# Kernel optimization log

Hardware: AMD Instinct MI355X
Metric: run time of the kernel (lower is better)

The kernel has to match this reference:

```python
import jax, jax.numpy as jnp
import numpy as np

EMBED_DIM = 128
N_EMBED = 10000
INPUT_SHAPE = (8, 64, 32, EMBED_DIM)


def setup_inputs() -> dict:
    key = jax.random.key(0)
    k1, k2 = jax.random.split(key)
    inputs = jax.random.normal(k1, INPUT_SHAPE, dtype=jnp.float32)
    cluster_mean = jax.random.normal(k2, (EMBED_DIM, N_EMBED), dtype=jnp.float32)
    return {"inputs": inputs, "cluster_mean": cluster_mean}


def reference(inputs, cluster_mean):
    embed_dim = cluster_mean.shape[0]
    # Flatten all leading dims: (N, D)
    samples = inputs.reshape(-1, embed_dim)
    # Squared euclidean distance to each code: (N, n_embed)
    dist = (
        jnp.sum(samples ** 2, axis=1, keepdims=True)
        - 2.0 * samples @ cluster_mean
        + jnp.sum(cluster_mean ** 2, axis=0, keepdims=True)
    )
    cluster_index = jnp.argmin(dist, axis=1).reshape(inputs.shape[:-1])
    # Embedding lookup from transposed codebook: (..., D)
    quantize = cluster_mean.T[cluster_index]
    q_loss = jnp.mean((quantize - jax.lax.stop_gradient(inputs)) ** 2)
    e_loss = jnp.mean((jax.lax.stop_gradient(quantize) - inputs) ** 2)
    loss = q_loss + 0.25 * e_loss
    # Straight-through estimator
    outputs = inputs + jax.lax.stop_gradient(quantize - inputs)
    return outputs, loss
```

## Files before the change

### kernel.cpp

```cpp
#include <hip/hip_runtime.h>

#define EMBED 128
#define NCODE 10000
#define NSAMP 16384
#define NCODE_PAD 10240
#define NSPLIT 8
#define SPLIT_CODES 1280
#define NCHUNK 20
#define CHUNK_ELEMS 8192
#define OUT_ELEMS (NSAMP * EMBED)
#define TAU 0.002f
#define NSEG 16

typedef float f32x16 __attribute__((ext_vector_type(16)));
typedef short s16x8 __attribute__((ext_vector_type(8)));
typedef unsigned short ushort_t;
typedef unsigned long long u64;

#define OFF_AH  0
#define OFF_AL  2621440
#define OFF_CT  5242880
#define OFF_CN  10485760
#define OFF_KEY 10526720
#define OFF_C2  11575296
#define OFF_IDX 12099584
#define OFF_RL  12165120
#define OFF_CNT 12230656
#define OFF_BEST 12230720

__device__ __forceinline__ unsigned short f2bf(float f) {
    unsigned u = __float_as_uint(f);
    return (unsigned short)((u + 0x7fffu + ((u >> 16) & 1u)) >> 16);
}
__device__ __forceinline__ float bf2f(unsigned short h) {
    return __uint_as_float(((unsigned)h) << 16);
}
__device__ __forceinline__ unsigned ordf(float f) {
    unsigned u = __float_as_uint(f);
    return (u & 0x80000000u) ? ~u : (u | 0x80000000u);
}
__device__ __forceinline__ float unordf(unsigned o) {
    return __uint_as_float((o & 0x80000000u) ? (o ^ 0x80000000u) : ~o);
}

__global__ __launch_bounds__(256) void prep_all(const float* __restrict__ C,
                                                ushort_t* __restrict__ Ah,
                                                ushort_t* __restrict__ Al,
                                                float* __restrict__ CT,
                                                float* __restrict__ cnorm,
                                                float* __restrict__ out,
                                                int* __restrict__ counter) {
    __shared__ float red[256];
    const int t  = threadIdx.x;
    const int nl = t & 15;
    const int kg = t >> 4;
    const int n  = blockIdx.x * 16 + nl;
    if (blockIdx.x == 0 && t == 0) { out[OUT_ELEMS] = 0.f; *counter = 0; }

    const int split = n / SPLIT_CODES;
    const int rem   = n % SPLIT_CODES;
    const int chunk = rem >> 6;
    const int mb    = (rem >> 5) & 1;
    const int row   = rem & 31;
    const int ks = kg >> 1, kh = kg & 1;
    const size_t eoff = (size_t)(split * NCHUNK + chunk) * CHUNK_ELEMS
                      + (size_t)(mb * 4096 + (ks * 2 + kh) * 256 + row * 8);
    const int k0 = kg * 8;
    float f[8];
    float s = 0.f;
#pragma unroll
    for (int j = 0; j < 8; ++j) {
        f[j] = (n < NCODE) ? C[(size_t)(k0 + j) * NCODE + n] : 0.f;
        s = fmaf(f[j], f[j], s);
    }
    *(float4*)(CT + (size_t)n * EMBED + k0)     = make_float4(f[0], f[1], f[2], f[3]);
    *(float4*)(CT + (size_t)n * EMBED + k0 + 4) = make_float4(f[4], f[5], f[6], f[7]);
    s16x8 vh, vl;
#pragma unroll
    for (int j = 0; j < 8; ++j) {
        unsigned short h = f2bf(f[j]);
        vh[j] = (short)h;
        vl[j] = (short)f2bf(f[j] - bf2f(h));
    }
    *(s16x8*)(Ah + eoff) = vh;
    *(s16x8*)(Al + eoff) = vl;

    red[t] = s;
    __syncthreads();
    if (t < 128) red[t] += red[t + 128];
    __syncthreads();
    if (t < 64) red[t] += red[t + 64];
    __syncthreads();
    if (t < 32) red[t] += red[t + 32];
    __syncthreads();
    if (t < 16) {
        const int nn = blockIdx.x * 16 + t;
        cnorm[nn] = (nn < NCODE) ? (red[t] + red[t + 16]) : 3.0e38f;
    }
}

__global__ __launch_bounds__(256, 2) void vq7(const float* __restrict__ X,
                                              const ushort_t* __restrict__ Ah,
                                              const ushort_t* __restrict__ Al,
                                              const float* __restrict__ cnorm,
                                              u64* __restrict__ candKey,
                                              unsigned* __restrict__ cand2) {
    __shared__ ushort_t Bs[2 * 2 * CHUNK_ELEMS];
    __shared__ __align__(16) float cns[SPLIT_CODES];
    const int t    = threadIdx.x;
    const int lane = t & 63;
    const int wave = t >> 6;
    const int ln   = lane & 31;
    const int kh   = lane >> 5;
    const int split = blockIdx.y;
    const int m0    = blockIdx.x * 256;
    const int sbase = split * SPLIT_CODES;

    s16x8 bh[2][8], bl[2][8];
#pragma unroll
    for (int g = 0; g < 2; ++g) {
        int m = m0 + wave * 64 + g * 32 + ln;
#pragma unroll
        for (int ks = 0; ks < 8; ++ks) {
            const float* src = X + (size_t)m * EMBED + ks * 16 + kh * 8;
            float4 f0 = *(const float4*)src;
            float4 f1 = *(const float4*)(src + 4);
            float f[8] = {f0.x, f0.y, f0.z, f0.w, f1.x, f1.y, f1.z, f1.w};
            s16x8 vh, vl;
#pragma unroll
            for (int j = 0; j < 8; ++j) {
                float v = -2.f * f[j];
                unsigned short h = f2bf(v);
                vh[j] = (short)h;
                vl[j] = (short)f2bf(v - bf2f(h));
            }
            bh[g][ks] = vh;
            bl[g][ks] = vl;
        }
    }

    for (int i = t; i < SPLIT_CODES; i += 256) cns[i] = cnorm[sbase + i];

    float v1[2] = {3.4e38f, 3.4e38f}, v2[2] = {3.4e38f, 3.4e38f};
    int   j1[2] = {0, 0};

    auto ldsw = (__attribute__((address_space(3))) ushort_t*)Bs;
    const int woff = wave * 2048;
    const size_t chbase = (size_t)(split * NCHUNK) * CHUNK_ELEMS;

    auto stage = [&](int cc, int buf) {
        const size_t sb = chbase + (size_t)cc * CHUNK_ELEMS;
        const ushort_t* sh = Ah + sb + woff + lane * 8;
        const ushort_t* sl = Al + sb + woff + lane * 8;
        const int db = buf * 2 * CHUNK_ELEMS + woff;
#pragma unroll
        for (int i = 0; i < 4; ++i) {
            __builtin_amdgcn_global_load_lds(
                (const __attribute__((address_space(1))) void*)(sh + i * 512),
                (__attribute__((address_space(3))) void*)(ldsw + db + i * 512),
                16, 0, 0);
            __builtin_amdgcn_global_load_lds(
                (const __attribute__((address_space(1))) void*)(sl + i * 512),
                (__attribute__((address_space(3))) void*)(ldsw + db + CHUNK_ELEMS + i * 512),
                16, 0, 0);
        }
    };

#define MFMA_PHASE(BB, MB, CB2, P0, P1)                                       \
    {                                                                         \
        const float4 q0 = *(const float4*)&cns[(CB2)];                        \
        const float4 q1 = *(const float4*)&cns[(CB2) + 8];                    \
        const float4 q2 = *(const float4*)&cns[(CB2) + 16];                   \
        const float4 q3 = *(const float4*)&cns[(CB2) + 24];                   \
        P0 = (f32x16){q0.x, q0.y, q0.z, q0.w, q1.x, q1.y, q1.z, q1.w,         \
                      q2.x, q2.y, q2.z, q2.w, q3.x, q3.y, q3.z, q3.w};        \
        P1 = P0;                                                              \
        _Pragma("unroll")                                                     \
        for (int ks = 0; ks < 8; ++ks) {                                      \
            const int fo = (BB) + (MB) * 4096 + (ks * 2 + kh) * 256 + ln * 8; \
            s16x8 a_h = *(const s16x8*)&Bs[fo];                               \
            s16x8 a_l = *(const s16x8*)&Bs[CHUNK_ELEMS + fo];                 \
            P0 = __builtin_amdgcn_mfma_f32_32x32x16_bf16(a_h, bh[0][ks], P0, 0, 0, 0); \
            P1 = __builtin_amdgcn_mfma_f32_32x32x16_bf16(a_h, bh[1][ks], P1, 0, 0, 0); \
            P0 = __builtin_amdgcn_mfma_f32_32x32x16_bf16(a_h, bl[0][ks], P0, 0, 0, 0); \
            P1 = __builtin_amdgcn_mfma_f32_32x32x16_bf16(a_h, bl[1][ks], P1, 0, 0, 0); \
            P0 = __builtin_amdgcn_mfma_f32_32x32x16_bf16(a_l, bh[0][ks], P0, 0, 0, 0); \
            P1 = __builtin_amdgcn_mfma_f32_32x32x16_bf16(a_l, bh[1][ks], P1, 0, 0, 0); \
        }                                                                     \
    }

#define EPI(P0, P1, CB2)                                                      \
    {                                                                         \
        _Pragma("unroll")                                                     \
        for (int r = 0; r < 16; ++r) {                                        \
            const int cc = (CB2) + ((r & 3) + 8 * (r >> 2));                  \
            const float d0 = P0[r];                                           \
            if (d0 < v1[0]) j1[0] = cc;                                       \
            v2[0] = fminf(v2[0], fmaxf(d0, v1[0]));                           \
            v1[0] = fminf(v1[0], d0);                                         \
            const float d1 = P1[r];                                           \
            if (d1 < v1[1]) j1[1] = cc;                                       \
            v2[1] = fminf(v2[1], fmaxf(d1, v1[1]));                           \
            v1[1] = fminf(v1[1], d1);                                         \
        }                                                                     \
    }

    f32x16 aA0, aA1, aB0, aB1;
    int cbA, cbB;

    stage(0, 0);
    __syncthreads();
    {
        stage(1, 1);
        const int cb = 4 * kh;
        MFMA_PHASE(0, 0, cb, aA0, aA1);
        cbA = cb;
        MFMA_PHASE(0, 1, cb + 32, aB0, aB1);
        EPI(aA0, aA1, cbA);
        cbB = cb + 32;
        __syncthreads();
    }

    for (int c = 1; c < NCHUNK; ++c) {
        const int b = c & 1;
        if (c + 1 < NCHUNK) stage(c + 1, 1 - b);
        const int bb = b * 2 * CHUNK_ELEMS;
        const int cb = c * 64 + 4 * kh;

        MFMA_PHASE(bb, 0, cb, aA0, aA1);
        EPI(aB0, aB1, cbB);
        cbA = cb;
        MFMA_PHASE(bb, 1, cb + 32, aB0, aB1);
        EPI(aA0, aA1, cbA);
        cbB = cb + 32;
        __syncthreads();
    }
    EPI(aB0, aB1, cbB);

#pragma unroll
    for (int g = 0; g < 2; ++g) {
        float ov1 = __shfl_xor(v1[g], 32, 64);
        int   oj1 = __shfl_xor(j1[g], 32, 64);
        float ov2 = __shfl_xor(v2[g], 32, 64);
        float hi = fmaxf(v1[g], ov1);
        v2[g] = fminf(fminf(v2[g], ov2), hi);
        if (ov1 < v1[g] || (ov1 == v1[g] && oj1 < j1[g])) { v1[g] = ov1; j1[g] = oj1; }
        if (kh == 0) {
            int m = m0 + wave * 64 + g * 32 + ln;
            candKey[(size_t)m * NSPLIT + split] =
                ((u64)ordf(v1[g]) << 32) | (unsigned)(sbase + j1[g]);
            cand2[(size_t)m * NSPLIT + split] = ordf(v2[g]);
        }
    }
#undef MFMA_PHASE
#undef EPI
}

__global__ __launch_bounds__(256) void outfin_k(const float* __restrict__ X,
                                                const float* __restrict__ CT,
                                                const u64* __restrict__ candKey,
                                                const unsigned* __restrict__ cand2,
                                                int* __restrict__ idxf,
                                                int* __restrict__ rlist,
                                                int* __restrict__ counter,
                                                u64* __restrict__ wsBest,
                                                float* __restrict__ out) {
    __shared__ float red[4];
    const int t = threadIdx.x;
    const int m = blockIdx.x * 8 + (t >> 5);
    const int l = t & 31;

    int code = 0;
    if (l == 0) {
        u64 best = 0xffffffffffffffffull;
        float v2 = 3.4e38f;
#pragma unroll
        for (int s = 0; s < NSPLIT; ++s) {
            u64 k = candKey[(size_t)m * NSPLIT + s];
            unsigned o2 = cand2[(size_t)m * NSPLIT + s];
            if (k < best) {
                if (best != 0xffffffffffffffffull)
                    v2 = fminf(v2, unordf((unsigned)(best >> 32)));
                best = k;
                v2 = fminf(v2, unordf(o2));
            } else {
                v2 = fminf(v2, unordf((unsigned)(k >> 32)));
            }
        }
        code = (int)(unsigned)(best & 0xffffffffu);
        idxf[m] = code;
        float v1 = unordf((unsigned)(best >> 32));
        if (v2 - v1 <= TAU) {
            rlist[atomicAdd(counter, 1)] = m;
            wsBest[m] = 0xffffffffffffffffull;
        }
    }
    code = __shfl(code, 0, 32);

    float4 q = *(const float4*)(CT + (size_t)code * EMBED + l * 4);
    float4 x = *(const float4*)(X + (size_t)m * EMBED + l * 4);
    *(float4*)(out + (size_t)m * EMBED + l * 4) = q;
    float dx = q.x - x.x, dy = q.y - x.y, dz = q.z - x.z, dw = q.w - x.w;
    float lsum = dx * dx + dy * dy + dz * dz + dw * dw;
#pragma unroll
    for (int off = 1; off < 64; off <<= 1) lsum += __shfl_xor(lsum, off, 64);
    if ((t & 63) == 0) red[t >> 6] = lsum;
    __syncthreads();
    if (t == 0)
        atomicAdd(out + OUT_ELEMS,
                  (red[0] + red[1] + red[2] + red[3]) * (1.25f / (float)OUT_ELEMS));
}

__global__ __launch_bounds__(256) void rescue_seg(const float* __restrict__ X,
                                                  const float* __restrict__ CT,
                                                  const float* __restrict__ cnorm,
                                                  const int* __restrict__ rlist,
                                                  const int* __restrict__ counter,
                                                  u64* __restrict__ wsBest) {
    __shared__ float xs[EMBED];
    __shared__ u64 wk[4];
    const int t = threadIdx.x;
    const int lane = t & 63;
    const int wave = t >> 6;
    const int hw = t & 31;
    const int slot = t >> 5;
    const int cnt = *counter;
    const int nw = cnt * NSEG;

    for (int w = blockIdx.x; w < nw; w += gridDim.x) {
        const int s = w >> 4, seg = w & 15;
        const int m = rlist[s];
        __syncthreads();
        if (t < 32) {
            float4 v = *(const float4*)(X + (size_t)m * EMBED + t * 4);
            xs[t * 4 + 0] = v.x; xs[t * 4 + 1] = v.y;
            xs[t * 4 + 2] = v.z; xs[t * 4 + 3] = v.w;
        }
        __syncthreads();
        const float x0 = xs[hw * 4 + 0], x1 = xs[hw * 4 + 1];
        const float x2 = xs[hw * 4 + 2], x3 = xs[hw * 4 + 3];
        const int base = seg * 625;
        const int jend = base + 625;
        u64 bk = 0xffffffffffffffffull;
        for (int it = 0; it < 20; ++it) {
            const int r0 = base + it * 32 + slot * 4;
            float4 c0, c1, c2, c3;
            bool ok0 = (r0 + 0 < jend), ok1 = (r0 + 1 < jend);
            bool ok2 = (r0 + 2 < jend), ok3 = (r0 + 3 < jend);
            c0 = ok0 ? *(const float4*)(CT + (size_t)(r0 + 0) * EMBED + hw * 4) : make_float4(0, 0, 0, 0);
            c1 = ok1 ? *(const float4*)(CT + (size_t)(r0 + 1) * EMBED + hw * 4) : make_float4(0, 0, 0, 0);
            c2 = ok2 ? *(const float4*)(CT + (size_t)(r0 + 2) * EMBED + hw * 4) : make_float4(0, 0, 0, 0);
            c3 = ok3 ? *(const float4*)(CT + (size_t)(r0 + 3) * EMBED + hw * 4) : make_float4(0, 0, 0, 0);
            float p0 = x0 * c0.x, p1 = x0 * c1.x, p2 = x0 * c2.x, p3 = x0 * c3.x;
            p0 = fmaf(x1, c0.y, p0); p1 = fmaf(x1, c1.y, p1);
            p2 = fmaf(x1, c2.y, p2); p3 = fmaf(x1, c3.y, p3);
            p0 = fmaf(x2, c0.z, p0); p1 = fmaf(x2, c1.z, p1);
            p2 = fmaf(x2, c2.z, p2); p3 = fmaf(x2, c3.z, p3);
            p0 = fmaf(x3, c0.w, p0); p1 = fmaf(x3, c1.w, p1);
            p2 = fmaf(x3, c2.w, p2); p3 = fmaf(x3, c3.w, p3);
#pragma unroll
            for (int off = 1; off < 32; off <<= 1) {
                p0 += __shfl_xor(p0, off, 32);
                p1 += __shfl_xor(p1, off, 32);
                p2 += __shfl_xor(p2, off, 32);
                p3 += __shfl_xor(p3, off, 32);
            }
            if (hw == 0) {
                if (ok0) { u64 k = ((u64)ordf(fmaf(-2.f, p0, cnorm[r0 + 0])) << 32) | (unsigned)(r0 + 0); if (k < bk) bk = k; }
                if (ok1) { u64 k = ((u64)ordf(fmaf(-2.f, p1, cnorm[r0 + 1])) << 32) | (unsigned)(r0 + 1); if (k < bk) bk = k; }
                if (ok2) { u64 k = ((u64)ordf(fmaf(-2.f, p2, cnorm[r0 + 2])) << 32) | (unsigned)(r0 + 2); if (k < bk) bk = k; }
                if (ok3) { u64 k = ((u64)ordf(fmaf(-2.f, p3, cnorm[r0 + 3])) << 32) | (unsigned)(r0 + 3); if (k < bk) bk = k; }
            }
        }
#pragma unroll
        for (int off = 1; off < 64; off <<= 1) {
            u64 o = __shfl_xor(bk, off, 64);
            if (o < bk) bk = o;
        }
        if (lane == 0) wk[wave] = bk;
        __syncthreads();
        if (t == 0) {
            u64 b = wk[0];
            if (wk[1] < b) b = wk[1];
            if (wk[2] < b) b = wk[2];
            if (wk[3] < b) b = wk[3];
            atomicMin(&wsBest[m], b);
        }
    }
}

__global__ __launch_bounds__(256) void patch_k(const float* __restrict__ X,
                                               const float* __restrict__ CT,
                                               const int* __restrict__ rlist,
                                               const int* __restrict__ counter,
                                               const u64* __restrict__ wsBest,
                                               const int* __restrict__ idxf,
                                               float* __restrict__ out) {
    const int t = threadIdx.x;
    const int l = t & 31, sl = t >> 5;
    const int cnt = *counter;
    for (int s = blockIdx.x * 8 + sl; s < cnt; s += gridDim.x * 8) {
        int m = rlist[s];
        u64 key = wsBest[m];
        int jn = (int)(unsigned)(key & 0xffffffffu);
        int jo = idxf[m];
        if (jn == jo) continue;
        float4 qn = *(const float4*)(CT + (size_t)jn * EMBED + l * 4);
        float4 qo = *(const float4*)(CT + (size_t)jo * EMBED + l * 4);
        float4 x  = *(const float4*)(X + (size_t)m * EMBED + l * 4);
        *(float4*)(out + (size_t)m * EMBED + l * 4) = qn;
        float dn = (qn.x - x.x) * (qn.x - x.x) + (qn.y - x.y) * (qn.y - x.y)
                 + (qn.z - x.z) * (qn.z - x.z) + (qn.w - x.w) * (qn.w - x.w);
        float dp = (qo.x - x.x) * (qo.x - x.x) + (qo.y - x.y) * (qo.y - x.y)
                 + (qo.z - x.z) * (qo.z - x.z) + (qo.w - x.w) * (qo.w - x.w);
        float delta = dn - dp;
#pragma unroll
        for (int off = 1; off < 32; off <<= 1) delta += __shfl_xor(delta, off, 32);
        if (l == 0)
            atomicAdd(out + OUT_ELEMS, delta * (1.25f / (float)OUT_ELEMS));
    }
}

extern "C" void kernel_launch(void* const* d_in, const int* in_sizes, int n_in,
                              void* d_out, int out_size, void* d_ws, size_t ws_size,
                              hipStream_t stream) {
    const float* X = (const float*)d_in[0];
    const float* C = (const float*)d_in[1];
    float* out = (float*)d_out;
    char* ws = (char*)d_ws;

    ushort_t* Ah = (ushort_t*)(ws + OFF_AH);
    ushort_t* Al = (ushort_t*)(ws + OFF_AL);
    float* CT    = (float*)(ws + OFF_CT);
    float* cnorm = (float*)(ws + OFF_CN);
    u64* candKey = (u64*)(ws + OFF_KEY);
    unsigned* cand2 = (unsigned*)(ws + OFF_C2);
    int* idxf    = (int*)(ws + OFF_IDX);
    int* rlist   = (int*)(ws + OFF_RL);
    int* counter = (int*)(ws + OFF_CNT);
    u64* wsBest  = (u64*)(ws + OFF_BEST);

    prep_all<<<NCODE_PAD / 16, 256, 0, stream>>>(C, Ah, Al, CT, cnorm, out, counter);
    vq7<<<dim3(NSAMP / 256, NSPLIT), 256, 0, stream>>>(X, Ah, Al, cnorm, candKey, cand2);
    outfin_k<<<NSAMP / 8, 256, 0, stream>>>(X, CT, candKey, cand2, idxf, rlist, counter, wsBest, out);
    rescue_seg<<<1024, 256, 0, stream>>>(X, CT, cnorm, rlist, counter, wsBest);
    patch_k<<<64, 256, 0, stream>>>(X, CT, rlist, counter, wsBest, idxf, out);
}
```

Before: 266.2 us.

## Zero-init MFMA accumulators, add code norm in epilogue, spread loss atomics

MFMA accumulators now start at zero instead of being seeded with code norms from LDS, and each code norm is added per element in the epilogue. MFMA phases are wrapped in s_setprio to favour the matrix work. The loss is accumulated into 64 separate slots and summed later in patch_k, and the output quantize write moves out of outfin_k into a new outwrite_k kernel. This adds a kernel launch and extra LDS reads and adds in the epilogue, in exchange for less atomic contention and possibly better MFMA scheduling.

```diff
diff --git a/kernel.cpp b/kernel.cpp
--- a/kernel.cpp
+++ b/kernel.cpp
@@ -27,6 +27,7 @@
 #define OFF_RL  12165120
 #define OFF_CNT 12230656
 #define OFF_BEST 12230720
+#define OFF_LOSS 12361792
 
 __device__ __forceinline__ unsigned short f2bf(float f) {
     unsigned u = __float_as_uint(f);
@@ -49,13 +50,17 @@
                                                 float* __restrict__ CT,
                                                 float* __restrict__ cnorm,
                                                 float* __restrict__ out,
-                                                int* __restrict__ counter) {
+                                                int* __restrict__ counter,
+                                                float* __restrict__ lossbuf) {
     __shared__ float red[256];
     const int t  = threadIdx.x;
     const int nl = t & 15;
     const int kg = t >> 4;
     const int n  = blockIdx.x * 16 + nl;
-    if (blockIdx.x == 0 && t == 0) { out[OUT_ELEMS] = 0.f; *counter = 0; }
+    if (blockIdx.x == 0) {
+        if (t == 0) { out[OUT_ELEMS] = 0.f; *counter = 0; }
+        if (t < 64) lossbuf[t] = 0.f;
+    }
 
     const int split = n / SPLIT_CODES;
     const int rem   = n % SPLIT_CODES;
@@ -106,7 +111,7 @@
                                               u64* __restrict__ candKey,
                                               unsigned* __restrict__ cand2) {
     __shared__ ushort_t Bs[2 * 2 * CHUNK_ELEMS];
-    __shared__ __align__(16) float cns[SPLIT_CODES];
+    __shared__ float cns[SPLIT_CODES];
     const int t    = threadIdx.x;
     const int lane = t & 63;
     const int wave = t >> 6;
@@ -166,15 +171,11 @@
         }
     };
 
-#define MFMA_PHASE(BB, MB, CB2, P0, P1)                                       \
+#define MFMA_PHASE(BB, MB, P0, P1)                                            \
     {                                                                         \
-        const float4 q0 = *(const float4*)&cns[(CB2)];                        \
-        const float4 q1 = *(const float4*)&cns[(CB2) + 8];                    \
-        const float4 q2 = *(const float4*)&cns[(CB2) + 16];                   \
-        const float4 q3 = *(const float4*)&cns[(CB2) + 24];                   \
-        P0 = (f32x16){q0.x, q0.y, q0.z, q0.w, q1.x, q1.y, q1.z, q1.w,         \
-                      q2.x, q2.y, q2.z, q2.w, q3.x, q3.y, q3.z, q3.w};        \
-        P1 = P0;                                                              \
+        P0 = (f32x16){0,0,0,0,0,0,0,0,0,0,0,0,0,0,0,0};                       \
+        P1 = (f32x16){0,0,0,0,0,0,0,0,0,0,0,0,0,0,0,0};                       \
+        __builtin_amdgcn_s_setprio(1);                                        \
         _Pragma("unroll")                                                     \
         for (int ks = 0; ks < 8; ++ks) {                                      \
             const int fo = (BB) + (MB) * 4096 + (ks * 2 + kh) * 256 + ln * 8; \
@@ -187,20 +188,22 @@
             P0 = __builtin_amdgcn_mfma_f32_32x32x16_bf16(a_l, bh[0][ks], P0, 0, 0, 0); \
             P1 = __builtin_amdgcn_mfma_f32_32x32x16_bf16(a_l, bh[1][ks], P1, 0, 0, 0); \
         }                                                                     \
-    }
-
-#define EPI(P0, P1, CB2)                                                      \
+        __builtin_amdgcn_s_setprio(0);                                        \
+    }
+
+#define EPI(P0, P1, CB)                                                       \
     {                                                                         \
         _Pragma("unroll")                                                     \
         for (int r = 0; r < 16; ++r) {                                        \
-            const int cc = (CB2) + ((r & 3) + 8 * (r >> 2));                  \
-            const float d0 = P0[r];                                           \
+            const int cc = (CB) + ((r & 3) + 8 * (r >> 2));                   \
+            const float cn = cns[cc];                                         \
+            float d0 = P0[r] + cn;                                            \
+            v2[0] = fminf(v2[0], fmaxf(d0, v1[0]));                           \
             if (d0 < v1[0]) j1[0] = cc;                                       \
-            v2[0] = fminf(v2[0], fmaxf(d0, v1[0]));                           \
             v1[0] = fminf(v1[0], d0);                                         \
-            const float d1 = P1[r];                                           \
+            float d1 = P1[r] + cn;                                            \
+            v2[1] = fminf(v2[1], fmaxf(d1, v1[1]));                           \
             if (d1 < v1[1]) j1[1] = cc;                                       \
-            v2[1] = fminf(v2[1], fmaxf(d1, v1[1]));                           \
             v1[1] = fminf(v1[1], d1);                                         \
         }                                                                     \
     }
@@ -213,9 +216,9 @@
     {
         stage(1, 1);
         const int cb = 4 * kh;
-        MFMA_PHASE(0, 0, cb, aA0, aA1);
+        MFMA_PHASE(0, 0, aA0, aA1);
         cbA = cb;
-        MFMA_PHASE(0, 1, cb + 32, aB0, aB1);
+        MFMA_PHASE(0, 1, aB0, aB1);
         EPI(aA0, aA1, cbA);
         cbB = cb + 32;
         __syncthreads();
@@ -227,10 +230,10 @@
         const int bb = b * 2 * CHUNK_ELEMS;
         const int cb = c * 64 + 4 * kh;
 
-        MFMA_PHASE(bb, 0, cb, aA0, aA1);
+        MFMA_PHASE(bb, 0, aA0, aA1);
         EPI(aB0, aB1, cbB);
         cbA = cb;
-        MFMA_PHASE(bb, 1, cb + 32, aB0, aB1);
+        MFMA_PHASE(bb, 1, aB0, aB1);
         EPI(aA0, aA1, cbA);
         cbB = cb + 32;
         __syncthreads();
@@ -264,7 +267,7 @@
                                                 int* __restrict__ rlist,
                                                 int* __restrict__ counter,
                                                 u64* __restrict__ wsBest,
-                                                float* __restrict__ out) {
+                                                float* __restrict__ lossbuf) {
     __shared__ float red[4];
     const int t = threadIdx.x;
     const int m = blockIdx.x * 8 + (t >> 5);
@@ -297,9 +300,11 @@
     }
     code = __shfl(code, 0, 32);
 
+    const float* X2 = X;
     float4 q = *(const float4*)(CT + (size_t)code * EMBED + l * 4);
-    float4 x = *(const float4*)(X + (size_t)m * EMBED + l * 4);
-    *(float4*)(out + (size_t)m * EMBED + l * 4) = q;
+    float4 x = *(const float4*)(X2 + (size_t)m * EMBED + l * 4);
+    float* out = lossbuf - (OFF_LOSS - 0) / 4;
+    (void)out;
     float dx = q.x - x.x, dy = q.y - x.y, dz = q.z - x.z, dw = q.w - x.w;
     float lsum = dx * dx + dy * dy + dz * dz + dw * dw;
 #pragma unroll
@@ -307,8 +312,20 @@
     if ((t & 63) == 0) red[t >> 6] = lsum;
     __syncthreads();
     if (t == 0)
-        atomicAdd(out + OUT_ELEMS,
+        atomicAdd(&lossbuf[blockIdx.x & 63],
                   (red[0] + red[1] + red[2] + red[3]) * (1.25f / (float)OUT_ELEMS));
+}
+
+__global__ __launch_bounds__(256) void outwrite_k(const float* __restrict__ X,
+                                                  const float* __restrict__ CT,
+                                                  const int* __restrict__ idxf,
+                                                  float* __restrict__ out) {
+    const int t = threadIdx.x;
+    const int m = blockIdx.x * 8 + (t >> 5);
+    const int l = t & 31;
+    const int code = idxf[m];
+    float4 q = *(const float4*)(CT + (size_t)code * EMBED + l * 4);
+    *(float4*)(out + (size_t)m * EMBED + l * 4) = q;
 }
 
 __global__ __launch_bounds__(256) void rescue_seg(const float* __restrict__ X,
@@ -395,9 +412,16 @@
                                                const int* __restrict__ counter,
                                                const u64* __restrict__ wsBest,
                                                const int* __restrict__ idxf,
+                                               const float* __restrict__ lossbuf,
                                                float* __restrict__ out) {
     const int t = threadIdx.x;
     const int l = t & 31, sl = t >> 5;
+    if (blockIdx.x == 0 && t == 0) {
+        float s = 0.f;
+#pragma unroll
+        for (int i = 0; i < 64; ++i) s += lossbuf[i];
+        atomicAdd(out + OUT_ELEMS, s);
+    }
     const int cnt = *counter;
     for (int s = blockIdx.x * 8 + sl; s < cnt; s += gridDim.x * 8) {
         int m = rlist[s];
@@ -439,10 +463,12 @@
     int* rlist   = (int*)(ws + OFF_RL);
     int* counter = (int*)(ws + OFF_CNT);
     u64* wsBest  = (u64*)(ws + OFF_BEST);
-
-    prep_all<<<NCODE_PAD / 16, 256, 0, stream>>>(C, Ah, Al, CT, cnorm, out, counter);
+    float* lossbuf = (float*)(ws + OFF_LOSS);
+
+    prep_all<<<NCODE_PAD / 16, 256, 0, stream>>>(C, Ah, Al, CT, cnorm, out, counter, lossbuf);
     vq7<<<dim3(NSAMP / 256, NSPLIT), 256, 0, stream>>>(X, Ah, Al, cnorm, candKey, cand2);
-    outfin_k<<<NSAMP / 8, 256, 0, stream>>>(X, CT, candKey, cand2, idxf, rlist, counter, wsBest, out);
+    outfin_k<<<NSAMP / 8, 256, 0, stream>>>(X, CT, candKey, cand2, idxf, rlist, counter, wsBest, lossbuf);
+    outwrite_k<<<NSAMP / 8, 256, 0, stream>>>(X, CT, idxf, out);
     rescue_seg<<<1024, 256, 0, stream>>>(X, CT, cnorm, rlist, counter, wsBest);
-    patch_k<<<64, 256, 0, stream>>>(X, CT, rlist, counter, wsBest, idxf, out);
-}
+    patch_k<<<64, 256, 0, stream>>>(X, CT, rlist, counter, wsBest, idxf, lossbuf, out);
+}
```

Measured after the change: 254.5 us. 4.4% less time.
